# Kernel optimization log

Hardware: AMD Instinct MI355X
Metric: run time of the kernel (lower is better)

The kernel has to match this reference:

```python
import jax, jax.numpy as jnp
import numpy as np

H = 64        # hidden_dim
T = 3         # message passing steps
M = 3         # set2set steps
NEF = 4       # num_edge_features
NNF = 11      # num_node_features
NT = 12       # num_targets
N_NODES = 10000
N_EDGES = 50000
B = 256       # number of graphs


def setup_inputs() -> dict:
    key = jax.random.key(0)
    ks = jax.random.split(key, 32)

    def p(k, shape):
        fan_in = shape[-1]
        return jax.random.normal(k, shape, jnp.float32) / np.sqrt(fan_in)

    inp = {}
    inp['x'] = jax.random.normal(ks[0], (N_NODES, NNF), jnp.float32)
    inp['edge_attr'] = jax.random.uniform(ks[1], (N_EDGES, NEF), jnp.float32)
    inp['edge_index'] = jax.random.randint(ks[2], (2, N_EDGES), 0, N_NODES)
    inp['batch'] = jnp.sort(jax.random.randint(ks[3], (N_NODES,), 0, B))
    inp['batch_size'] = B
    # nn1: edge MLP -> per-edge HxH weight
    inp['w1a'] = p(ks[4], (H, NEF)); inp['b1a'] = jnp.zeros((H,), jnp.float32)
    inp['w1b'] = p(ks[5], (H, H));   inp['b1b'] = jnp.zeros((H,), jnp.float32)
    inp['w1c'] = p(ks[6], (H * H, H)); inp['b1c'] = jnp.zeros((H * H,), jnp.float32)
    # GRUCell
    inp['gru_wih'] = p(ks[7], (3 * H, H)); inp['gru_whh'] = p(ks[8], (3 * H, H))
    inp['gru_bih'] = jnp.zeros((3 * H,), jnp.float32); inp['gru_bhh'] = jnp.zeros((3 * H,), jnp.float32)
    # lin: (H + NNF) -> 2H
    inp['lin_w'] = p(ks[9], (2 * H, H + NNF)); inp['lin_b'] = jnp.zeros((2 * H,), jnp.float32)
    # Set2Set 2-layer LSTM: in_channels = 2H, input = 4H, hidden = 2H
    IC = 2 * H
    inp['lstm_wih0'] = p(ks[10], (4 * IC, 2 * IC)); inp['lstm_whh0'] = p(ks[11], (4 * IC, IC))
    inp['lstm_bih0'] = jnp.zeros((4 * IC,), jnp.float32); inp['lstm_bhh0'] = jnp.zeros((4 * IC,), jnp.float32)
    inp['lstm_wih1'] = p(ks[12], (4 * IC, IC)); inp['lstm_whh1'] = p(ks[13], (4 * IC, IC))
    inp['lstm_bih1'] = jnp.zeros((4 * IC,), jnp.float32); inp['lstm_bhh1'] = jnp.zeros((4 * IC,), jnp.float32)
    # nn2: 4H -> 8H -> num_targets
    inp['w2a'] = p(ks[14], (8 * H, 4 * H)); inp['b2a'] = jnp.zeros((8 * H,), jnp.float32)
    inp['w2b'] = p(ks[15], (NT, 8 * H)); inp['b2b'] = jnp.zeros((NT,), jnp.float32)
    return inp


def _gru(x, h, wih, whh, bih, bhh):
    gi = x @ wih.T + bih
    gh = h @ whh.T + bhh
    ir, iz, inn = jnp.split(gi, 3, axis=1)
    hr, hz, hn = jnp.split(gh, 3, axis=1)
    r = jax.nn.sigmoid(ir + hr)
    z = jax.nn.sigmoid(iz + hz)
    n = jnp.tanh(inn + r * hn)
    return (1.0 - z) * n + z * h


def _lstm(x, h, c, wih, whh, bih, bhh):
    g = x @ wih.T + bih + h @ whh.T + bhh
    i, f, gg, o = jnp.split(g, 4, axis=1)
    c_new = jax.nn.sigmoid(f) * c + jax.nn.sigmoid(i) * jnp.tanh(gg)
    h_new = jax.nn.sigmoid(o) * jnp.tanh(c_new)
    return h_new, c_new


def reference(x, edge_attr, w1a, b1a, w1b, b1b, w1c, b1c,
              gru_wih, gru_whh, gru_bih, gru_bhh, lin_w, lin_b,
              lstm_wih0, lstm_whh0, lstm_bih0, lstm_bhh0,
              lstm_wih1, lstm_whh1, lstm_bih1, lstm_bhh1,
              w2a, b2a, w2b, b2b, edge_index, batch, batch_size):
    N = x.shape[0]
    E = edge_attr.shape[0]
    src, dst = edge_index[0], edge_index[1]

    # pad node features into hidden state
    h = jnp.zeros((N, H), x.dtype).at[:, :x.shape[1]].set(x)

    # nn1 edge MLP -> per-edge (H, H) weight (edge_attr constant over T, hoisted)
    e1 = jax.nn.relu(edge_attr @ w1a.T + b1a)
    e1 = jax.nn.relu(e1 @ w1b.T + b1b)
    W_edge = (e1 @ w1c.T + b1c).reshape(E, H, H)  # [E, in, out]

    # T rounds of NNConv (gather -> per-edge matvec -> scatter-add) + GRU
    for _ in range(T):
        m_e = jnp.einsum('eh,eho->eo', h[src], W_edge)
        m = jax.ops.segment_sum(m_e, dst, num_segments=N)
        h = _gru(m, h, gru_wih, gru_whh, gru_bih, gru_bhh)

    h = jnp.concatenate([h, x], axis=1) @ lin_w.T + lin_b  # [N, 2H]

    # Set2Set readout with 2-layer LSTM
    IC = 2 * H
    q_star = jnp.zeros((batch_size, 2 * IC), h.dtype)
    h0 = jnp.zeros((batch_size, IC), h.dtype); c0 = jnp.zeros_like(h0)
    h1 = jnp.zeros_like(h0); c1 = jnp.zeros_like(h0)
    for _ in range(M):
        h0, c0 = _lstm(q_star, h0, c0, lstm_wih0, lstm_whh0, lstm_bih0, lstm_bhh0)
        h1, c1 = _lstm(h0, h1, c1, lstm_wih1, lstm_whh1, lstm_bih1, lstm_bhh1)
        q = h1  # [B, IC]
        e = jnp.sum(h * q[batch], axis=-1)  # [N]
        emax = jax.ops.segment_max(e, batch, num_segments=batch_size)
        a = jnp.exp(e - emax[batch])
        denom = jax.ops.segment_sum(a, batch, num_segments=batch_size)
        a = a / denom[batch]
        r = jax.ops.segment_sum(a[:, None] * h, batch, num_segments=batch_size)
        q_star = jnp.concatenate([q, r], axis=-1)  # [B, 4H]

    out = jax.nn.relu(q_star @ w2a.T + b2a) @ w2b.T + b2b
    return out
```

## Files before the change

kernel.cpp:

```cpp
#include <hip/hip_runtime.h>
#include <math.h>

#define NN 10000
#define NE 50000
#define BG 256
#define NNF 11
#define NT 12

typedef unsigned int u32;
typedef __attribute__((ext_vector_type(8))) short short8v;
typedef __attribute__((ext_vector_type(4))) float f32x4;

__device__ __forceinline__ float sigm(float x){ return 1.0f/(1.0f+__expf(-x)); }
__device__ __forceinline__ u32 f2bf(float f){
  u32 u = __float_as_uint(f);
  return (u + 0x7fffu + ((u>>16)&1u)) >> 16;
}
__device__ __forceinline__ float bf2f(u32 s){ return __uint_as_float(s<<16); }

__global__ void k_h_init(const float* __restrict__ x, float* __restrict__ h,
                         unsigned short* __restrict__ hHi, unsigned short* __restrict__ hLo){
  int tid = blockIdx.x*256 + threadIdx.x;
  if (tid >= NN*64) return;
  int n = tid >> 6, j = tid & 63;
  float v = (j < NNF) ? x[n*NNF + j] : 0.0f;
  h[tid] = v;
  u32 hv = f2bf(v);
  hHi[tid] = (unsigned short)hv;
  hLo[tid] = (unsigned short)f2bf(v - bf2f(hv));
}

__global__ void k_prep(const float* __restrict__ gwih, const float* __restrict__ gwhh,
                       const float* __restrict__ linw, const float* __restrict__ w1b,
                       const float* __restrict__ wih0, const float* __restrict__ whh0,
                       const float* __restrict__ wih1, const float* __restrict__ whh1,
                       const float* __restrict__ w2a,  const float* __restrict__ w1c,
                       float* __restrict__ wihT, float* __restrict__ whhT,
                       float* __restrict__ linT, unsigned short* __restrict__ w1bB,
                       float* __restrict__ wih0T, float* __restrict__ whh0T,
                       float* __restrict__ wih1T, float* __restrict__ whh1T,
                       float* __restrict__ w2aT, unsigned short* __restrict__ qtT,
                       int* __restrict__ deg, float* __restrict__ state0){
  int tid = blockIdx.x*256 + threadIdx.x;
  if (tid < 12288){ int i=tid>>6, j=tid&63; wihT[j*192+i]=gwih[tid]; return; }
  tid -= 12288;
  if (tid < 12288){ int i=tid>>6, j=tid&63; whhT[j*192+i]=gwhh[tid]; return; }
  tid -= 12288;
  if (tid < 9600){ int i=tid/75, j=tid-i*75; linT[j*128+i]=linw[tid]; return; }
  tid -= 9600;
  if (tid < 4096){ w1bB[tid] = (unsigned short)f2bf(w1b[tid]); return; }
  tid -= 4096;
  if (tid < 131072){ int i=tid>>8, j=tid&255; wih0T[j*512+i]=wih0[tid]; return; }
  tid -= 131072;
  if (tid < 65536){ int i=tid>>7, j=tid&127; whh0T[j*512+i]=whh0[tid]; return; }
  tid -= 65536;
  if (tid < 65536){ int i=tid>>7, j=tid&127; wih1T[j*512+i]=wih1[tid]; return; }
  tid -= 65536;
  if (tid < 65536){ int i=tid>>7, j=tid&127; whh1T[j*512+i]=whh1[tid]; return; }
  tid -= 65536;
  if (tid < 131072){ int i=tid>>8, j=tid&255; w2aT[j*512+i]=w2a[tid]; return; }
  tid -= 131072;
  if (tid < 262144){ int ko=tid>>6, hh=tid&63; int k=ko>>6, o=ko&63;
                     qtT[tid] = (unsigned short)f2bf(w1c[(hh*64+o)*64+k]); return; }
  tid -= 262144;
  if (tid < NN){ deg[tid] = 0; return; }
  tid -= NN;
  if (tid < 196608) state0[tid] = 0.f;
}

__global__ __launch_bounds__(256) void k_e1m(const float* __restrict__ ea,
                     const float* __restrict__ w1a, const float* __restrict__ b1a,
                     const unsigned short* __restrict__ w1bB, const float* __restrict__ b1b,
                     unsigned short* __restrict__ e1b){
  __shared__ unsigned short sHi[4][16][64], sLo[4][16][64];
  int t = threadIdx.x, w = t>>6, l = t&63;
  int c = l & 15, g = l >> 4;
  int eb = blockIdx.x*64 + w*16;
  float wa0=w1a[l*4+0], wa1=w1a[l*4+1], wa2=w1a[l*4+2], wa3=w1a[l*4+3];
  float bb1 = b1a[l];
  char* hbase = (char*)&sHi[w][0][0];
  char* lbase = (char*)&sLo[w][0][0];
  #pragma unroll
  for (int r = 0; r < 16; ++r){
    int e = eb + r; if (e >= NE) e = NE-1;
    float4 a = *(const float4*)&ea[e*4];
    float h1 = fmaxf(bb1 + a.x*wa0 + a.y*wa1 + a.z*wa2 + a.w*wa3, 0.f);
    u32 hv = f2bf(h1);
    u32 lv = f2bf(h1 - bf2f(hv));
    int wb = (r*128 + l*2) ^ ((r & 7) << 4);
    *(unsigned short*)(hbase + wb) = (unsigned short)hv;
    *(unsigned short*)(lbase + wb) = (unsigned short)lv;
  }
  __syncthreads();
  int xv = (c & 7) << 4;
  int rb0 = (c*128 + g*16) ^ xv;
  int rb1 = (c*128 + 64 + g*16) ^ xv;
  short8v aH0 = *(const short8v*)(hbase + rb0);
  short8v aH1 = *(const short8v*)(hbase + rb1);
  short8v aL0 = *(const short8v*)(lbase + rb0);
  short8v aL1 = *(const short8v*)(lbase + rb1);
  f32x4 acc[4];
  #pragma unroll
  for (int f = 0; f < 4; ++f){
    const short* wrow = (const short*)w1bB + (f*16 + c)*64 + g*8;
    short8v b0 = *(const short8v*)wrow;
    short8v b1 = *(const short8v*)(wrow + 32);
    acc[f] = f32x4{0.f,0.f,0.f,0.f};
    acc[f] = __builtin_amdgcn_mfma_f32_16x16x32_bf16(aH0, b0, acc[f], 0, 0, 0);
    acc[f] = __builtin_amdgcn_mfma_f32_16x16x32_bf16(aL0, b0, acc[f], 0, 0, 0);
    acc[f] = __builtin_amdgcn_mfma_f32_16x16x32_bf16(aH1, b1, acc[f], 0, 0, 0);
    acc[f] = __builtin_amdgcn_mfma_f32_16x16x32_bf16(aL1, b1, acc[f], 0, 0, 0);
  }
  #pragma unroll
  for (int f = 0; f < 4; ++f){
    float bb2 = b1b[f*16 + c];
    #pragma unroll
    for (int r = 0; r < 4; ++r){
      int e = eb + 4*g + r;
      if (e < NE)
        e1b[e*64 + f*16 + c] = (unsigned short)f2bf(fmaxf(acc[f][r] + bb2, 0.f));
    }
  }
}

__global__ void k_hb(const float* __restrict__ h, const float* __restrict__ b1c,
                     float* __restrict__ hb, float* __restrict__ m){
  int tid = blockIdx.x*256 + threadIdx.x;
  int n = tid >> 6, o = tid & 63;
  const float* hr = h + n*64;
  float acc = 0.f;
  #pragma unroll 8
  for (int i = 0; i < 64; ++i) acc = fmaf(hr[i], b1c[i*64 + o], acc);
  hb[tid] = acc;
  m[tid] = 0.f;
}

__global__ __launch_bounds__(512) void k_P3(const unsigned short* __restrict__ hHi,
                      const unsigned short* __restrict__ hLo,
                      const unsigned short* __restrict__ qtT, u32* __restrict__ P2){
  __shared__ unsigned short sB[16384];
  int t = threadIdx.x; int w = t >> 6; int l = t & 63;
  int c = l & 15, g = l >> 4;
  int nt = blockIdx.x >> 4, kt = blockIdx.x & 15;
  int kob = kt*256;
  const char* qsrc = (const char*)qtT + (size_t)kob*128;
  char* sb = (char*)sB;
  #pragma unroll
  for (int r = 0; r < 4; ++r){
    int dstb = (r*512 + t)*16;
    int srcb = dstb ^ (((dstb >> 7) & 7) << 4);
    *(uint4*)(sb + dstb) = *(const uint4*)(qsrc + srcb);
  }
  int nb = nt*128 + w*16;
  int rowA = nb + c; if (rowA >= NN) rowA = NN-1;
  const short8v* aHiP = (const short8v*)((const short*)hHi + rowA*64 + g*8);
  const short8v* aLoP = (const short8v*)((const short*)hLo + rowA*64 + g*8);
  short8v aH0 = aHiP[0], aH1 = aHiP[4];
  short8v aL0 = aLoP[0], aL1 = aLoP[4];
  __syncthreads();
  int xv = (c & 7) << 4;
  f32x4 acc[16];
  #pragma unroll
  for (int f = 0; f < 16; ++f) acc[f] = f32x4{0.f,0.f,0.f,0.f};
  #pragma unroll
  for (int f = 0; f < 16; ++f){
    int baseb = f*2048 + c*128 + g*16;
    short8v b0 = *(const short8v*)(sb + (baseb ^ xv));
    short8v b1 = *(const short8v*)(sb + ((baseb + 64) ^ xv));
    acc[f] = __builtin_amdgcn_mfma_f32_16x16x32_bf16(aH0, b0, acc[f], 0, 0, 0);
    acc[f] = __builtin_amdgcn_mfma_f32_16x16x32_bf16(aL0, b0, acc[f], 0, 0, 0);
    acc[f] = __builtin_amdgcn_mfma_f32_16x16x32_bf16(aH1, b1, acc[f], 0, 0, 0);
    acc[f] = __builtin_amdgcn_mfma_f32_16x16x32_bf16(aL1, b1, acc[f], 0, 0, 0);
  }
  int k2b = kt*2;
  #pragma unroll
  for (int r = 0; r < 4; ++r){
    int node = nb + 4*g + r;
    if (node < NN){
      u32* dst = P2 + (size_t)node*2048;
      #pragma unroll
      for (int kk = 0; kk < 2; ++kk){
        uint4 v;
        v.x = f2bf(acc[8*kk+0][r]) | (f2bf(acc[8*kk+4][r]) << 16);
        v.y = f2bf(acc[8*kk+1][r]) | (f2bf(acc[8*kk+5][r]) << 16);
        v.z = f2bf(acc[8*kk+2][r]) | (f2bf(acc[8*kk+6][r]) << 16);
        v.w = f2bf(acc[8*kk+3][r]) | (f2bf(acc[8*kk+7][r]) << 16);
        *(uint4*)(dst + (k2b+kk)*64 + c*4) = v;
      }
    }
  }
}

__global__ void k_deg(const int* __restrict__ ei, int* __restrict__ deg){
  int e = blockIdx.x*256 + threadIdx.x;
  if (e >= NE) return;
  atomicAdd(&deg[ei[e]], 1);
}

__global__ __launch_bounds__(256) void k_scan(const int* __restrict__ deg, int* __restrict__ rowptr,
                       int* __restrict__ cursor){
  __shared__ int part[256];
  int t = threadIdx.x;
  int base = t*40;
  int s = 0;
  for (int i = 0; i < 40; ++i){ int idx = base+i; if (idx < NN) s += deg[idx]; }
  part[t] = s;
  __syncthreads();
  for (int off = 1; off < 256; off <<= 1){
    int v = (t >= off) ? part[t-off] : 0;
    __syncthreads();
    part[t] += v;
    __syncthreads();
  }
  int run = (t == 0) ? 0 : part[t-1];
  for (int i = 0; i < 40; ++i){
    int idx = base+i;
    if (idx < NN){ rowptr[idx] = run; cursor[idx] = run; run += deg[idx]; }
  }
  if (t == 255) rowptr[NN] = part[255];
}

__global__ void k_fill(const int* __restrict__ ei, int* __restrict__ cursor, int* __restrict__ csr_e){
  int e = blockIdx.x*256 + threadIdx.x;
  if (e >= NE) return;
  int s = ei[e];
  int pos = atomicAdd(&cursor[s], 1);
  csr_e[pos] = e;
}

__global__ __launch_bounds__(256) void k_msg2(const int* __restrict__ rowptr, const int* __restrict__ csr_e,
                       const int* __restrict__ ei, const u32* __restrict__ e1u,
                       const u32* __restrict__ P2, const float* __restrict__ hb,
                       float* __restrict__ m){
  int t = threadIdx.x; int w = t >> 6; int l = t & 63;
  int oo = ((l & 3) << 4) | (l >> 2);
  int n = blockIdx.x*4 + w;
  int jb = rowptr[n], je = rowptr[n+1];
  if (jb == je) return;
  float hbv = hb[n*64 + oo];
  const u32* Pn = P2 + (size_t)n*2048;
  u32 pr[32];
  #pragma unroll
  for (int k2 = 0; k2 < 32; ++k2) pr[k2] = Pn[k2*64 + l];
  for (int j = jb; j < je; ++j){
    int e = csr_e[j];
    int dst = ei[NE + e];
    const u32* er = e1u + e*32;
    float acc = hbv;
    #pragma unroll 8
    for (int k2 = 0; k2 < 32; ++k2){
      u32 ew = er[k2];
      u32 pv = pr[k2];
      acc = fmaf(bf2f(ew & 0xffffu), bf2f(pv & 0xffffu), acc);
      acc = fmaf(bf2f(ew >> 16),     bf2f(pv >> 16),     acc);
    }
    atomicAdd(&m[dst*64 + oo], acc);
  }
}

__global__ __launch_bounds__(256) void k_gru(const float* __restrict__ m, float* __restrict__ h,
                     unsigned short* __restrict__ hHi, unsigned short* __restrict__ hLo,
                     const float* __restrict__ wihT, const float* __restrict__ whhT,
                     const float* __restrict__ bih, const float* __restrict__ bhh){
  __shared__ float sm[8][64], sh[8][64];
  int t = threadIdx.x, w = t>>6, lane = t&63;
  int n0 = blockIdx.x*8 + w*2;
  sm[2*w][lane]   = m[n0*64+lane];
  sm[2*w+1][lane] = m[(n0+1)*64+lane];
  sh[2*w][lane]   = h[n0*64+lane];
  sh[2*w+1][lane] = h[(n0+1)*64+lane];
  __syncthreads();
  float gi[2][3] = {{0,0,0},{0,0,0}}, gh[2][3] = {{0,0,0},{0,0,0}};
  #pragma unroll 2
  for (int i=0;i<64;++i){
    const float* wr = wihT + i*192;
    const float* ur = whhT + i*192;
    float w0=wr[lane], w1=wr[64+lane], w2=wr[128+lane];
    float u0=ur[lane], u1=ur[64+lane], u2=ur[128+lane];
    #pragma unroll
    for (int q=0;q<2;++q){
      float mi = sm[2*w+q][i], hi = sh[2*w+q][i];
      gi[q][0]=fmaf(mi,w0,gi[q][0]); gi[q][1]=fmaf(mi,w1,gi[q][1]); gi[q][2]=fmaf(mi,w2,gi[q][2]);
      gh[q][0]=fmaf(hi,u0,gh[q][0]); gh[q][1]=fmaf(hi,u1,gh[q][1]); gh[q][2]=fmaf(hi,u2,gh[q][2]);
    }
  }
  #pragma unroll
  for (int q=0;q<2;++q){
    int n = n0 + q;
    float r  = sigm(gi[q][0]+bih[lane]      + gh[q][0]+bhh[lane]);
    float z  = sigm(gi[q][1]+bih[64+lane]   + gh[q][1]+bhh[64+lane]);
    float nn_= tanhf(gi[q][2]+bih[128+lane] + r*(gh[q][2]+bhh[128+lane]));
    float ho = sh[2*w+q][lane];
    float hv = (1.f-z)*nn_ + z*ho;
    h[n*64+lane] = hv;
    u32 hv16 = f2bf(hv);
    hHi[n*64+lane] = (unsigned short)hv16;
    hLo[n*64+lane] = (unsigned short)f2bf(hv - bf2f(hv16));
  }
}

__global__ __launch_bounds__(256) void k_lin(const float* __restrict__ h, const float* __restrict__ x,
                     const float* __restrict__ linT, const float* __restrict__ lin_b, float* __restrict__ h2){
  __shared__ float sh[4][64];
  int t=threadIdx.x, w=t>>6, lane=t&63;
  int n = blockIdx.x*4 + w;
  sh[w][lane] = h[n*64+lane];
  __syncthreads();
  float a0 = lin_b[lane], a1 = lin_b[64+lane];
  #pragma unroll 4
  for (int i=0;i<64;++i){
    float v = sh[w][i];
    a0 = fmaf(v, linT[i*128+lane], a0);
    a1 = fmaf(v, linT[i*128+64+lane], a1);
  }
  #pragma unroll
  for (int i=0;i<11;++i){
    float v = x[n*NNF+i];
    a0 = fmaf(v, linT[(64+i)*128+lane], a0);
    a1 = fmaf(v, linT[(64+i)*128+64+lane], a1);
  }
  h2[n*128+lane] = a0;
  h2[n*128+64+lane] = a1;
}

__global__ void k_bounds(const int* __restrict__ batch, int* __restrict__ gstart){
  int b = blockIdx.x*256 + threadIdx.x;
  if (b > BG) return;
  int lo=0, hi=NN;
  while (lo < hi){ int mid=(lo+hi)>>1; if (batch[mid] < b) lo=mid+1; else hi=mid; }
  gstart[b]=lo;
}

__global__ __launch_bounds__(512) void k_lstm01(
    float* __restrict__ qstar,
    float* __restrict__ h0, float* __restrict__ c0,
    float* __restrict__ h1, float* __restrict__ c1,
    const float* __restrict__ wih0T, const float* __restrict__ whh0T,
    const float* __restrict__ bih0, const float* __restrict__ bhh0,
    const float* __restrict__ wih1T, const float* __restrict__ whh1T,
    const float* __restrict__ bih1, const float* __restrict__ bhh1){
  __shared__ float sin[256], s0[128], s1[128], sg[512];
  int b = blockIdx.x, j = threadIdx.x;
  if (j < 256) sin[j] = qstar[b*256 + j];
  else if (j < 384) s0[j-256] = h0[b*128 + (j-256)];
  else s1[j-384] = h1[b*128 + (j-384)];
  __syncthreads();
  {
    float a0 = bih0[j] + bhh0[j], a1 = 0.f, a2 = 0.f, a3 = 0.f;
    #pragma unroll
    for (int i = 0; i < 256; i += 4){
      a0 = fmaf(sin[i],   wih0T[(i)*512+j],   a0);
      a1 = fmaf(sin[i+1], wih0T[(i+1)*512+j], a1);
      a2 = fmaf(sin[i+2], wih0T[(i+2)*512+j], a2);
      a3 = fmaf(sin[i+3], wih0T[(i+3)*512+j], a3);
    }
    #pragma unroll
    for (int i = 0; i < 128; i += 4){
      a0 = fmaf(s0[i],   whh0T[(i)*512+j],   a0);
      a1 = fmaf(s0[i+1], whh0T[(i+1)*512+j], a1);
      a2 = fmaf(s0[i+2], whh0T[(i+2)*512+j], a2);
      a3 = fmaf(s0[i+3], whh0T[(i+3)*512+j], a3);
    }
    sg[j] = (a0+a1)+(a2+a3);
  }
  __syncthreads();
  if (j < 128){
    float ig = sigm(sg[j]), fg = sigm(sg[128+j]);
    float gg = tanhf(sg[256+j]), og = sigm(sg[384+j]);
    float c = fg*c0[b*128+j] + ig*gg;
    c0[b*128+j] = c;
    float hh = og*tanhf(c);
    h0[b*128+j] = hh;
    s0[j] = hh;
  }
  __syncthreads();
  {
    float a0 = bih1[j] + bhh1[j], a1 = 0.f, a2 = 0.f, a3 = 0.f;
    #pragma unroll
    for (int i = 0; i < 128; i += 4){
      a0 = fmaf(s0[i],   wih1T[(i)*512+j],   a0);
      a1 = fmaf(s0[i+1], wih1T[(i+1)*512+j], a1);
      a2 = fmaf(s0[i+2], wih1T[(i+2)*512+j], a2);
      a3 = fmaf(s0[i+3], wih1T[(i+3)*512+j], a3);
    }
    #pragma unroll
    for (int i = 0; i < 128; i += 4){
      a0 = fmaf(s1[i],   whh1T[(i)*512+j],   a0);
      a1 = fmaf(s1[i+1], whh1T[(i+1)*512+j], a1);
      a2 = fmaf(s1[i+2], whh1T[(i+2)*512+j], a2);
      a3 = fmaf(s1[i+3], whh1T[(i+3)*512+j], a3);
    }
    sg[j] = (a0+a1)+(a2+a3);
  }
  __syncthreads();
  if (j < 128){
    float ig = sigm(sg[j]), fg = sigm(sg[128+j]);
    float gg = tanhf(sg[256+j]), og = sigm(sg[384+j]);
    float c = fg*c1[b*128+j] + ig*gg;
    c1[b*128+j] = c;
    float hh = og*tanhf(c);
    h1[b*128+j] = hh;
    qstar[b*256+j] = hh;
  }
}

__global__ __launch_bounds__(256) void k_attn2(const float* __restrict__ h2,
                       const float* __restrict__ h1,
                       const int* __restrict__ gstart, float* __restrict__ qstar){
  __shared__ float pm[4], pl[4], pr[4][128];
  int b = blockIdx.x, t = threadIdx.x, w = t>>6, lane = t&63;
  float q0 = h1[b*128+lane], q1 = h1[b*128+64+lane];
  int s = gstart[b], e = gstart[b+1];
  float mrun = -3.0e38f, l = 0.f, r0 = 0.f, r1 = 0.f;
  for (int n = s + w; n < e; n += 4){
    float v0 = h2[n*128+lane], v1 = h2[n*128+64+lane];
    float d = fmaf(v0, q0, v1*q1);
    #pragma unroll
    for (int off = 32; off; off >>= 1) d += __shfl_xor(d, off);
    float mn = fmaxf(mrun, d);
    float sc = __expf(mrun - mn);
    float ww = __expf(d - mn);
    l = l*sc + ww;
    r0 = r0*sc + ww*v0;
    r1 = r1*sc + ww*v1;
    mrun = mn;
  }
  pr[w][lane] = r0; pr[w][64+lane] = r1;
  if (lane == 0){ pm[w] = mrun; pl[w] = l; }
  __syncthreads();
  if (t < 128){
    float M = fmaxf(fmaxf(pm[0],pm[1]), fmaxf(pm[2],pm[3]));
    float L = 0.f, R = 0.f;
    #pragma unroll
    for (int ww = 0; ww < 4; ++ww){
      float sc = __expf(pm[ww] - M);
      L = fmaf(pl[ww], sc, L);
      R = fmaf(pr[ww][t], sc, R);
    }
    float inv = (L > 0.f) ? 1.f/L : 0.f;
    qstar[b*256 + 128 + t] = R*inv;
  }
}

__global__ __launch_bounds__(512) void k_head(const float* __restrict__ qstar,
                      const float* __restrict__ w2aT, const float* __restrict__ b2a,
                      const float* __restrict__ w2b,  const float* __restrict__ b2b,
                      float* __restrict__ out){
  __shared__ float qs[256], sg[512];
  int b = blockIdx.x, j = threadIdx.x, w = j>>6, lane = j&63;
  if (j < 256) qs[j] = qstar[b*256 + j];
  __syncthreads();
  float a0 = b2a[j], a1 = 0.f, a2 = 0.f, a3 = 0.f;
  #pragma unroll
  for (int i = 0; i < 256; i += 4){
    a0 = fmaf(qs[i],   w2aT[(i)*512+j],   a0);
    a1 = fmaf(qs[i+1], w2aT[(i+1)*512+j], a1);
    a2 = fmaf(qs[i+2], w2aT[(i+2)*512+j], a2);
    a3 = fmaf(qs[i+3], w2aT[(i+3)*512+j], a3);
  }
  sg[j] = fmaxf((a0+a1)+(a2+a3), 0.f);
  __syncthreads();
  for (int jj = w; jj < NT; jj += 8){
    const float* wr = w2b + jj*512;
    float acc = 0.f;
    #pragma unroll
    for (int i = 0; i < 8; ++i) acc = fmaf(sg[lane+i*64], wr[lane+i*64], acc);
    #pragma unroll
    for (int off = 32; off; off >>= 1) acc += __shfl_xor(acc, off);
    if (lane == 0) out[b*NT+jj] = acc + b2b[jj];
  }
}

extern "C" void kernel_launch(void* const* d_in, const int* in_sizes, int n_in,
                              void* d_out, int out_size, void* d_ws, size_t ws_size,
                              hipStream_t stream) {
  const float* x    = (const float*)d_in[0];
  const float* ea   = (const float*)d_in[1];
  const int*   eidx = (const int*)d_in[2];
  const int*   batch= (const int*)d_in[3];
  const float* w1a  = (const float*)d_in[5];
  const float* b1a  = (const float*)d_in[6];
  const float* w1b  = (const float*)d_in[7];
  const float* b1b  = (const float*)d_in[8];
  const float* w1c  = (const float*)d_in[9];
  const float* b1c  = (const float*)d_in[10];
  const float* gwih = (const float*)d_in[11];
  const float* gwhh = (const float*)d_in[12];
  const float* gbih = (const float*)d_in[13];
  const float* gbhh = (const float*)d_in[14];
  const float* linw = (const float*)d_in[15];
  const float* linb = (const float*)d_in[16];
  const float* wih0 = (const float*)d_in[17];
  const float* whh0 = (const float*)d_in[18];
  const float* bih0 = (const float*)d_in[19];
  const float* bhh0 = (const float*)d_in[20];
  const float* wih1 = (const float*)d_in[21];
  const float* whh1 = (const float*)d_in[22];
  const float* bih1 = (const float*)d_in[23];
  const float* bhh1 = (const float*)d_in[24];
  const float* w2a  = (const float*)d_in[25];
  const float* b2a  = (const float*)d_in[26];
  const float* w2b  = (const float*)d_in[27];
  const float* b2b  = (const float*)d_in[28];
  float* out = (float*)d_out;

  char* p = (char*)d_ws;
  auto alloc = [&](size_t nbytes){ void* r = (void*)p; p += (nbytes + 255) & ~size_t(255); return r; };
  float* h    = (float*)alloc((size_t)NN*64*4);
  float* hb   = (float*)alloc((size_t)NN*64*4);
  float* m    = (float*)alloc((size_t)NN*64*4);
  float* h2   = (float*)alloc((size_t)NN*128*4);
  float* wihT = (float*)alloc(64*192*4);
  float* whhT = (float*)alloc(64*192*4);
  float* linT = (float*)alloc(75*128*4);
  unsigned short* w1bB = (unsigned short*)alloc(64*64*2);
  float* wih0T= (float*)alloc(256*512*4);
  float* whh0T= (float*)alloc(128*512*4);
  float* wih1T= (float*)alloc(128*512*4);
  float* whh1T= (float*)alloc(128*512*4);
  float* w2aT = (float*)alloc(256*512*4);
  float* qstar= (float*)alloc(256*256*4);
  float* h0   = (float*)alloc(256*128*4);
  float* c0   = (float*)alloc(256*128*4);
  float* h1s  = (float*)alloc(256*128*4);
  float* c1   = (float*)alloc(256*128*4);
  int*  gstart= (int*)alloc(257*4);
  unsigned short* e1b = (unsigned short*)alloc((size_t)NE*64*2);
  unsigned short* qtT = (unsigned short*)alloc((size_t)4096*64*2);
  unsigned short* hHi = (unsigned short*)alloc((size_t)NN*64*2);
  unsigned short* hLo = (unsigned short*)alloc((size_t)NN*64*2);
  int*  deg   = (int*)alloc((size_t)NN*4);
  int*  rowptr= (int*)alloc((size_t)(NN+1)*4);
  int*  cursor= (int*)alloc((size_t)NN*4);
  int*  csr_e = (int*)alloc((size_t)NE*4);
  u32*  P2    = (u32*)alloc((size_t)NN*2048*4);

  k_prep<<<3773, 256, 0, stream>>>(gwih, gwhh, linw, w1b, wih0, whh0, wih1, whh1,
                                   w2a, w1c, wihT, whhT, linT, w1bB, wih0T, whh0T,
                                   wih1T, whh1T, w2aT, qtT, deg, qstar);
  k_h_init<<<2500, 256, 0, stream>>>(x, h, hHi, hLo);
  k_e1m<<<782, 256, 0, stream>>>(ea, w1a, b1a, w1bB, b1b, e1b);
  k_bounds<<<2, 256, 0, stream>>>(batch, gstart);
  k_deg<<<196, 256, 0, stream>>>(eidx, deg);
  k_scan<<<1, 256, 0, stream>>>(deg, rowptr, cursor);
  k_fill<<<196, 256, 0, stream>>>(eidx, cursor, csr_e);

  for (int t = 0; t < 3; ++t) {
    k_hb<<<2500, 256, 0, stream>>>(h, b1c, hb, m);
    k_P3<<<79*16, 512, 0, stream>>>(hHi, hLo, qtT, P2);
    k_msg2<<<2500, 256, 0, stream>>>(rowptr, csr_e, eidx, (const u32*)e1b, P2, hb, m);
    k_gru<<<1250, 256, 0, stream>>>(m, h, hHi, hLo, wihT, whhT, gbih, gbhh);
  }

  k_lin<<<2500, 256, 0, stream>>>(h, x, linT, linb, h2);

  for (int s = 0; s < 3; ++s) {
    k_lstm01<<<256, 512, 0, stream>>>(qstar, h0, c0, h1s, c1,
                                      wih0T, whh0T, bih0, bhh0,
                                      wih1T, whh1T, bih1, bhh1);
    k_attn2<<<256, 256, 0, stream>>>(h2, h1s, gstart, qstar);
  }

  k_head<<<256, 512, 0, stream>>>(qstar, w2aT, b2a, w2b, b2b, out);
}
```

Before: 556.3 us.

## Fuse hb/m-zero into GRU and init, prefetch edge rows in message kernel

The per-step k_hb kernel is removed. Its work (h·b1c projection and zeroing of m) is folded into k_h_init for the first step and into the tail of k_gru for later steps, which saves a launch and a re-read of h each iteration. The message kernel now loads each edge's bf16 row as eight uint4 vector loads and prefetches the next edge's row while the current one is processed. It splits the dot product over four accumulators and adds an occupancy hint through launch_bounds. In exchange, the last GRU step computes an unused hb, and the prefetch buffers raise register pressure.

```diff
diff --git a/kernel.cpp b/kernel.cpp
--- a/kernel.cpp
+++ b/kernel.cpp
@@ -18,16 +18,33 @@
 }
 __device__ __forceinline__ float bf2f(u32 s){ return __uint_as_float(s<<16); }
 
-__global__ void k_h_init(const float* __restrict__ x, float* __restrict__ h,
-                         unsigned short* __restrict__ hHi, unsigned short* __restrict__ hLo){
-  int tid = blockIdx.x*256 + threadIdx.x;
-  if (tid >= NN*64) return;
-  int n = tid >> 6, j = tid & 63;
-  float v = (j < NNF) ? x[n*NNF + j] : 0.0f;
-  h[tid] = v;
-  u32 hv = f2bf(v);
-  hHi[tid] = (unsigned short)hv;
-  hLo[tid] = (unsigned short)f2bf(v - bf2f(hv));
+__global__ __launch_bounds__(256) void k_h_init(const float* __restrict__ x, float* __restrict__ h,
+                         unsigned short* __restrict__ hHi, unsigned short* __restrict__ hLo,
+                         const float* __restrict__ b1c, float* __restrict__ hb,
+                         float* __restrict__ m){
+  __shared__ float sv[8][64];
+  int t = threadIdx.x, w = t>>6, lane = t&63;
+  int n0 = blockIdx.x*8 + w*2;
+  #pragma unroll
+  for (int q = 0; q < 2; ++q){
+    int n = n0 + q;
+    float v = (lane < NNF) ? x[n*NNF + lane] : 0.0f;
+    h[n*64+lane] = v;
+    u32 hv = f2bf(v);
+    hHi[n*64+lane] = (unsigned short)hv;
+    hLo[n*64+lane] = (unsigned short)f2bf(v - bf2f(hv));
+    sv[2*w+q][lane] = v;
+  }
+  __syncthreads();
+  #pragma unroll
+  for (int q = 0; q < 2; ++q){
+    int n = n0 + q;
+    float acc = 0.f;
+    #pragma unroll 8
+    for (int i = 0; i < 64; ++i) acc = fmaf(sv[2*w+q][i], b1c[i*64+lane], acc);
+    hb[n*64+lane] = acc;
+    m[n*64+lane] = 0.f;
+  }
 }
 
 __global__ void k_prep(const float* __restrict__ gwih, const float* __restrict__ gwhh,
@@ -123,18 +140,6 @@
   }
 }
 
-__global__ void k_hb(const float* __restrict__ h, const float* __restrict__ b1c,
-                     float* __restrict__ hb, float* __restrict__ m){
-  int tid = blockIdx.x*256 + threadIdx.x;
-  int n = tid >> 6, o = tid & 63;
-  const float* hr = h + n*64;
-  float acc = 0.f;
-  #pragma unroll 8
-  for (int i = 0; i < 64; ++i) acc = fmaf(hr[i], b1c[i*64 + o], acc);
-  hb[tid] = acc;
-  m[tid] = 0.f;
-}
-
 __global__ __launch_bounds__(512) void k_P3(const unsigned short* __restrict__ hHi,
                       const unsigned short* __restrict__ hLo,
                       const unsigned short* __restrict__ qtT, u32* __restrict__ P2){
@@ -228,7 +233,8 @@
   csr_e[pos] = e;
 }
 
-__global__ __launch_bounds__(256) void k_msg2(const int* __restrict__ rowptr, const int* __restrict__ csr_e,
+__global__ __launch_bounds__(256, 2) void k_msg3(const int* __restrict__ rowptr,
+                       const int* __restrict__ csr_e,
                        const int* __restrict__ ei, const u32* __restrict__ e1u,
                        const u32* __restrict__ P2, const float* __restrict__ hb,
                        float* __restrict__ m){
@@ -242,27 +248,48 @@
   u32 pr[32];
   #pragma unroll
   for (int k2 = 0; k2 < 32; ++k2) pr[k2] = Pn[k2*64 + l];
+  int e = csr_e[jb];
+  uint4 q[8];
+  {
+    const uint4* er4 = (const uint4*)(e1u + (size_t)e*32);
+    #pragma unroll
+    for (int i = 0; i < 8; ++i) q[i] = er4[i];
+  }
   for (int j = jb; j < je; ++j){
-    int e = csr_e[j];
     int dst = ei[NE + e];
-    const u32* er = e1u + e*32;
-    float acc = hbv;
-    #pragma unroll 8
-    for (int k2 = 0; k2 < 32; ++k2){
-      u32 ew = er[k2];
-      u32 pv = pr[k2];
-      acc = fmaf(bf2f(ew & 0xffffu), bf2f(pv & 0xffffu), acc);
-      acc = fmaf(bf2f(ew >> 16),     bf2f(pv >> 16),     acc);
-    }
-    atomicAdd(&m[dst*64 + oo], acc);
+    int en = (j+1 < je) ? csr_e[j+1] : e;
+    uint4 qn[8];
+    const uint4* ern = (const uint4*)(e1u + (size_t)en*32);
+    #pragma unroll
+    for (int i = 0; i < 8; ++i) qn[i] = ern[i];
+    float a0 = hbv, a1 = 0.f, a2 = 0.f, a3 = 0.f;
+    #pragma unroll
+    for (int i = 0; i < 8; ++i){
+      u32 w0 = q[i].x, w1 = q[i].y, w2 = q[i].z, w3 = q[i].w;
+      u32 p0 = pr[4*i], p1 = pr[4*i+1], p2 = pr[4*i+2], p3 = pr[4*i+3];
+      a0 = fmaf(bf2f(w0 & 0xffffu), bf2f(p0 & 0xffffu), a0);
+      a0 = fmaf(bf2f(w0 >> 16),     bf2f(p0 >> 16),     a0);
+      a1 = fmaf(bf2f(w1 & 0xffffu), bf2f(p1 & 0xffffu), a1);
+      a1 = fmaf(bf2f(w1 >> 16),     bf2f(p1 >> 16),     a1);
+      a2 = fmaf(bf2f(w2 & 0xffffu), bf2f(p2 & 0xffffu), a2);
+      a2 = fmaf(bf2f(w2 >> 16),     bf2f(p2 >> 16),     a2);
+      a3 = fmaf(bf2f(w3 & 0xffffu), bf2f(p3 & 0xffffu), a3);
+      a3 = fmaf(bf2f(w3 >> 16),     bf2f(p3 >> 16),     a3);
+    }
+    atomicAdd(&m[dst*64 + oo], (a0+a1)+(a2+a3));
+    #pragma unroll
+    for (int i = 0; i < 8; ++i) q[i] = qn[i];
+    e = en;
   }
 }
 
 __global__ __launch_bounds__(256) void k_gru(const float* __restrict__ m, float* __restrict__ h,
                      unsigned short* __restrict__ hHi, unsigned short* __restrict__ hLo,
                      const float* __restrict__ wihT, const float* __restrict__ whhT,
-                     const float* __restrict__ bih, const float* __restrict__ bhh){
-  __shared__ float sm[8][64], sh[8][64];
+                     const float* __restrict__ bih, const float* __restrict__ bhh,
+                     const float* __restrict__ b1c, float* __restrict__ hb,
+                     float* __restrict__ mz){
+  __shared__ float sm[8][64], sh[8][64], sv[8][64];
   int t = threadIdx.x, w = t>>6, lane = t&63;
   int n0 = blockIdx.x*8 + w*2;
   sm[2*w][lane]   = m[n0*64+lane];
@@ -296,6 +323,17 @@
     u32 hv16 = f2bf(hv);
     hHi[n*64+lane] = (unsigned short)hv16;
     hLo[n*64+lane] = (unsigned short)f2bf(hv - bf2f(hv16));
+    sv[2*w+q][lane] = hv;
+  }
+  __syncthreads();
+  #pragma unroll
+  for (int q=0;q<2;++q){
+    int n = n0 + q;
+    float acc = 0.f;
+    #pragma unroll 8
+    for (int i = 0; i < 64; ++i) acc = fmaf(sv[2*w+q][i], b1c[i*64+lane], acc);
+    hb[n*64+lane] = acc;
+    mz[n*64+lane] = 0.f;
   }
 }
 
@@ -538,7 +576,7 @@
   k_prep<<<3773, 256, 0, stream>>>(gwih, gwhh, linw, w1b, wih0, whh0, wih1, whh1,
                                    w2a, w1c, wihT, whhT, linT, w1bB, wih0T, whh0T,
                                    wih1T, whh1T, w2aT, qtT, deg, qstar);
-  k_h_init<<<2500, 256, 0, stream>>>(x, h, hHi, hLo);
+  k_h_init<<<1250, 256, 0, stream>>>(x, h, hHi, hLo, b1c, hb, m);
   k_e1m<<<782, 256, 0, stream>>>(ea, w1a, b1a, w1bB, b1b, e1b);
   k_bounds<<<2, 256, 0, stream>>>(batch, gstart);
   k_deg<<<196, 256, 0, stream>>>(eidx, deg);
@@ -546,10 +584,9 @@
   k_fill<<<196, 256, 0, stream>>>(eidx, cursor, csr_e);
 
   for (int t = 0; t < 3; ++t) {
-    k_hb<<<2500, 256, 0, stream>>>(h, b1c, hb, m);
     k_P3<<<79*16, 512, 0, stream>>>(hHi, hLo, qtT, P2);
-    k_msg2<<<2500, 256, 0, stream>>>(rowptr, csr_e, eidx, (const u32*)e1b, P2, hb, m);
-    k_gru<<<1250, 256, 0, stream>>>(m, h, hHi, hLo, wihT, whhT, gbih, gbhh);
+    k_msg3<<<2500, 256, 0, stream>>>(rowptr, csr_e, eidx, (const u32*)e1b, P2, hb, m);
+    k_gru<<<1250, 256, 0, stream>>>(m, h, hHi, hLo, wihT, whhT, gbih, gbhh, b1c, hb, m);
   }
 
   k_lin<<<2500, 256, 0, stream>>>(h, x, linT, linb, h2);
```

After: 508.0 us. -8.7%, faster.
